# Optimization experiments

Measured on AMD Instinct MI355X. Metric: run time of the kernel, lower is better.

Reference implementation:

```python
import jax, jax.numpy as jnp
import numpy as np

EMBED_DIM = 1024
HEADS = 16
HEAD_DIM = EMBED_DIM // HEADS


def setup_inputs() -> dict:
    key = jax.random.key(0)
    ks = jax.random.split(key, 9)
    B, T, C = 4, 4096, EMBED_DIM
    s = 1.0 / np.sqrt(C)
    inp = {
        "x": jax.random.normal(ks[0], (B, T, C), dtype=jnp.float32),
        "Wq": jax.random.normal(ks[1], (C, C), dtype=jnp.float32) * s,
        "bq": jnp.zeros((C,), dtype=jnp.float32),
        "Wk": jax.random.normal(ks[2], (C, C), dtype=jnp.float32) * s,
        "bk": jnp.zeros((C,), dtype=jnp.float32),
        "Wv": jax.random.normal(ks[3], (C, C), dtype=jnp.float32) * s,
        "bv": jnp.zeros((C,), dtype=jnp.float32),
        "Wc": jax.random.normal(ks[4], (C, C), dtype=jnp.float32) * s,
        "bc": jnp.zeros((C,), dtype=jnp.float32),
    }
    return inp


def reference(x, Wq, bq, Wk, bk, Wv, bv, Wc, bc):
    B, T, C = x.shape
    H, D = HEADS, HEAD_DIM
    # projections (torch Linear: x @ W.T + b)
    q = (x @ Wq.T + bq).reshape(B, T, H, D).transpose(0, 2, 1, 3)  # [B,H,T,D]
    k = (x @ Wk.T + bk).reshape(B, T, H, D).transpose(0, 2, 1, 3)
    v = (x @ Wv.T + bv).reshape(B, T, H, D).transpose(0, 2, 1, 3)
    # ELU+1 feature map
    q = jax.nn.elu(q) + 1.0
    k = jax.nn.elu(k) + 1.0
    # kv outer product: [B,H,D,D]
    kv = jnp.einsum("bhtd,bhte->bhde", k, v)
    # normalizer: q @ sum_t k  -> [B,H,T,1]
    k_sum = k.sum(axis=2)  # [B,H,D]
    z = 1.0 / (jnp.einsum("bhtd,bhd->bht", q, k_sum)[..., None] + 1e-6)
    y = jnp.einsum("bhtd,bhde->bhte", q, kv) * z  # [B,H,T,D]
    y = y.transpose(0, 2, 1, 3).reshape(B, T, C)
    return y @ Wc.T + bc
```

## Files before the change

kernel.cpp:

```cpp
#include <hip/hip_runtime.h>
#include <math.h>

#define EMBED 1024
#define HEADS 16
#define HD 64
#define BATCH 4
#define TSEQ 4096
#define BH (BATCH * HEADS)
#define MROWS (BATCH * TSEQ)

typedef _Float16 f16;
typedef __attribute__((ext_vector_type(4))) _Float16 f16x4;
typedef __attribute__((ext_vector_type(8))) _Float16 f16x8;
typedef __attribute__((ext_vector_type(4))) float f32x4;

#define GLOBAL_AS __attribute__((address_space(1)))
#define LDS_AS __attribute__((address_space(3)))

__device__ __forceinline__ float elu1(float v) {
    return v > 0.f ? v + 1.f : __expf(v);
}

__device__ __forceinline__ int swzc(int row, int col, int cols) {
    int g = (col >> 3) ^ (row & 7);
    return row * cols + (g << 3) + (col & 7);
}

__device__ __forceinline__ f16x8 fragld(const f16* t, int row, int k, int cols) {
    return *(const f16x8*)&t[swzc(row, k, cols)];
}

__device__ __forceinline__ f32x4 mfma16(f16x8 a, f16x8 b, f32x4 c) {
    return __builtin_amdgcn_mfma_f32_16x16x32_f16(a, b, c, 0, 0, 0);
}

__device__ __forceinline__ void gld_lds16(const f16* g, f16* l) {
    __builtin_amdgcn_global_load_lds((const GLOBAL_AS void*)g, (LDS_AS void*)l, 16, 0, 0);
}

__global__ __launch_bounds__(256) void prep(
    const float* __restrict__ x, f16* __restrict__ xh,
    const float* __restrict__ Wq, const float* __restrict__ Wk,
    const float* __restrict__ Wv, const float* __restrict__ Wc,
    const float* __restrict__ bq, const float* __restrict__ bk,
    const float* __restrict__ bv, const float* __restrict__ bc,
    f16* __restrict__ Wall, float* __restrict__ ball, float* __restrict__ kvz)
{
    int bid = blockIdx.x;
    if (bid < 16384) {
        size_t i4 = (size_t)bid * 256 + threadIdx.x;
        float4 f = *(const float4*)&x[i4 * 4];
        f16x4 h = {(f16)f.x, (f16)f.y, (f16)f.z, (f16)f.w};
        *(f16x4*)&xh[i4 * 4] = h;
    } else {
        int i4 = (bid - 16384) * 256 + threadIdx.x;
        int cls = i4 >> 18;
        const float* W = cls == 0 ? Wq : cls == 1 ? Wk : cls == 2 ? Wv : Wc;
        int off = (i4 & 0x3FFFF) * 4;
        float4 f = *(const float4*)&W[off];
        f16x4 h = {(f16)f.x, (f16)f.y, (f16)f.z, (f16)f.w};
        *(f16x4*)&Wall[(size_t)i4 * 4] = h;
        if (i4 < 4096) {
            int c2 = i4 >> 10;
            const float* bb = c2 == 0 ? bq : c2 == 1 ? bk : c2 == 2 ? bv : bc;
            ball[i4] = bb[i4 & 1023];
        }
        if (i4 < 66560) {
            *(float4*)&kvz[i4 * 4] = (float4){0.f, 0.f, 0.f, 0.f};
        }
    }
}

__global__ __launch_bounds__(256) void gemm_kv(
    const f16* __restrict__ xh, const f16* __restrict__ Wall,
    const float* __restrict__ ball,
    float* __restrict__ kvg, float* __restrict__ ksg)
{
    __shared__ __align__(16) f16 smem[2 * 128 * 64];
    f16* As = smem;
    f16* Bs = smem + 128 * 64;

    const int tid = threadIdx.x, lane = tid & 63, w = tid >> 6;
    const int wr = w >> 1, wc4 = w & 1, l15 = lane & 15, l4 = lane >> 4;

    const int m0 = blockIdx.x * 128;
    const int h = blockIdx.y;

    const int gcol = ((lane & 7) ^ (lane >> 3)) << 3;
    const int rsub = lane >> 3;
    const size_t arow = (size_t)(m0 + w * 32 + rsub) * EMBED + gcol;

    const int wrow = w * 32 + rsub;
    const int brow_idx = (wrow < 64) ? (1024 + h * 64 + wrow)
                                     : (2048 + h * 64 + (wrow - 64));
    const size_t brow = (size_t)brow_idx * EMBED + gcol;

    f32x4 acc[4][4];
    #pragma unroll
    for (int i = 0; i < 4; ++i)
        #pragma unroll
        for (int j = 0; j < 4; ++j) acc[i][j] = (f32x4){0.f, 0.f, 0.f, 0.f};

    for (int k0 = 0; k0 < EMBED; k0 += 64) {
        #pragma unroll
        for (int c = 0; c < 4; ++c) {
            gld_lds16(&xh[arow + (size_t)c * 8 * EMBED + k0], &As[(w * 4 + c) * 512]);
            gld_lds16(&Wall[brow + (size_t)c * 8 * EMBED + k0], &Bs[(w * 4 + c) * 512]);
        }
        __syncthreads();
        #pragma unroll
        for (int kk = 0; kk < 64; kk += 32) {
            f16x8 af[4], bf[4];
            #pragma unroll
            for (int i = 0; i < 4; ++i)
                af[i] = fragld(As, wr * 64 + i * 16 + l15, kk + l4 * 8, 64);
            #pragma unroll
            for (int j = 0; j < 4; ++j)
                bf[j] = fragld(Bs, wc4 * 64 + j * 16 + l15, kk + l4 * 8, 64);
            #pragma unroll
            for (int i = 0; i < 4; ++i)
                #pragma unroll
                for (int j = 0; j < 4; ++j)
                    acc[i][j] = mfma16(af[i], bf[j], acc[i][j]);
        }
        __syncthreads();
    }

    f16* kt = As;
    f16* vt = Bs;
    const float* biasp = ball + (wc4 ? 2048 : 1024) + h * 64;
    #pragma unroll
    for (int j = 0; j < 4; ++j) {
        int d = j * 16 + l15;
        float bj = biasp[d];
        f16* dst = wc4 ? vt : kt;
        #pragma unroll
        for (int i = 0; i < 4; ++i) {
            int t0 = wr * 64 + i * 16 + l4 * 4;
            f16x4 hv;
            #pragma unroll
            for (int r = 0; r < 4; ++r) {
                float vv = acc[i][j][r] + bj;
                if (!wc4) vv = elu1(vv);
                hv[r] = (f16)vv;
            }
            *(f16x4*)&dst[swzc(d, t0, 128)] = hv;
        }
    }
    __syncthreads();

    f32x4 kvacc[4];
    #pragma unroll
    for (int j = 0; j < 4; ++j) kvacc[j] = (f32x4){0.f, 0.f, 0.f, 0.f};
    #pragma unroll
    for (int tc = 0; tc < 4; ++tc) {
        f16x8 a = fragld(vt, 16 * w + l15, tc * 32 + l4 * 8, 128);
        #pragma unroll
        for (int j = 0; j < 4; ++j) {
            f16x8 bfr = fragld(kt, j * 16 + l15, tc * 32 + l4 * 8, 128);
            kvacc[j] = mfma16(a, bfr, kvacc[j]);
        }
    }
    float ksacc = 0.f;
    {
        int d = tid & 63, q4 = tid >> 6;
        #pragma unroll
        for (int t8 = 0; t8 < 32; t8 += 8) {
            f16x8 k8 = fragld(kt, d, q4 * 32 + t8, 128);
            #pragma unroll
            for (int e = 0; e < 8; ++e) ksacc += (float)k8[e];
        }
    }
    const int bh = (m0 >> 12) * HEADS + h;
    #pragma unroll
    for (int j = 0; j < 4; ++j)
        #pragma unroll
        for (int r = 0; r < 4; ++r)
            atomicAdd(&kvg[(size_t)bh * 4096 +
                           (size_t)(16 * w + l4 * 4 + r) * HD + j * 16 + l15],
                      kvacc[j][r]);
    atomicAdd(&ksg[bh * HD + (tid & 63)], ksacc);
}

__global__ __launch_bounds__(256) void gemm_qy(
    const f16* __restrict__ xh, const f16* __restrict__ Wall,
    const float* __restrict__ ball,
    const float* __restrict__ kvg, const float* __restrict__ ksg,
    f16* __restrict__ y)
{
    __shared__ __align__(16) f16 smem[2 * 128 * 64];
    __shared__ __align__(16) f16 kvs[2][64 * 64];
    __shared__ float kss[2][64];
    __shared__ float zs[128][2];
    f16* As = smem;
    f16* Bs = smem + 128 * 64;

    const int tid = threadIdx.x, lane = tid & 63, w = tid >> 6;
    const int wr = w >> 1, wc4 = w & 1, l15 = lane & 15, l4 = lane >> 4;

    const int m0 = blockIdx.x * 128;
    const int ny = blockIdx.y;
    const int n0 = ny * 128;
    const int bh0 = (m0 >> 12) * HEADS + 2 * ny;

    const int gcol = ((lane & 7) ^ (lane >> 3)) << 3;
    const int rsub = lane >> 3;
    const size_t arow = (size_t)(m0 + w * 32 + rsub) * EMBED + gcol;
    const size_t brow = (size_t)(n0 + w * 32 + rsub) * EMBED + gcol;

    f32x4 acc[4][4];
    #pragma unroll
    for (int i = 0; i < 4; ++i)
        #pragma unroll
        for (int j = 0; j < 4; ++j) acc[i][j] = (f32x4){0.f, 0.f, 0.f, 0.f};

    for (int k0 = 0; k0 < EMBED; k0 += 64) {
        #pragma unroll
        for (int c = 0; c < 4; ++c) {
            gld_lds16(&xh[arow + (size_t)c * 8 * EMBED + k0], &As[(w * 4 + c) * 512]);
            gld_lds16(&Wall[brow + (size_t)c * 8 * EMBED + k0], &Bs[(w * 4 + c) * 512]);
        }
        __syncthreads();
        #pragma unroll
        for (int kk = 0; kk < 64; kk += 32) {
            f16x8 af[4], bf[4];
            #pragma unroll
            for (int i = 0; i < 4; ++i)
                af[i] = fragld(As, wr * 64 + i * 16 + l15, kk + l4 * 8, 64);
            #pragma unroll
            for (int j = 0; j < 4; ++j)
                bf[j] = fragld(Bs, wc4 * 64 + j * 16 + l15, kk + l4 * 8, 64);
            #pragma unroll
            for (int i = 0; i < 4; ++i)
                #pragma unroll
                for (int j = 0; j < 4; ++j)
                    acc[i][j] = mfma16(af[i], bf[j], acc[i][j]);
        }
        __syncthreads();
    }

    #pragma unroll
    for (int c = 0; c < 8; ++c) {
        int idx = tid + c * 256;
        int hh = idx >> 10;
        int rem = idx & 1023;
        int e = rem >> 4, d4 = (rem & 15) << 2;
        float4 f = *(const float4*)&kvg[(size_t)(bh0 + hh) * 4096 + e * 64 + d4];
        f16x4 hv = {(f16)f.x, (f16)f.y, (f16)f.z, (f16)f.w};
        *(f16x4*)&kvs[hh][swzc(e, d4, 64)] = hv;
    }
    if (tid < 128) kss[tid >> 6][tid & 63] = ksg[(bh0 + (tid >> 6)) * HD + (tid & 63)];

    #pragma unroll
    for (int j = 0; j < 4; ++j) {
        int c = wc4 * 64 + j * 16 + l15;
        float bj = ball[n0 + c];
        #pragma unroll
        for (int i = 0; i < 4; ++i) {
            #pragma unroll
            for (int r = 0; r < 4; ++r) {
                int t = wr * 64 + i * 16 + l4 * 4 + r;
                smem[swzc(t, c, 128)] = (f16)elu1(acc[i][j][r] + bj);
            }
        }
    }
    __syncthreads();

    {
        int t = tid >> 1, hh = tid & 1;
        float s = 0.f;
        #pragma unroll
        for (int d8 = 0; d8 < 64; d8 += 8) {
            f16x8 qv = fragld(smem, t, hh * 64 + d8, 128);
            #pragma unroll
            for (int e = 0; e < 8; ++e) s += (float)qv[e] * kss[hh][d8 + e];
        }
        zs[t][hh] = 1.f / (s + 1e-6f);
    }

    const int hh = w >> 1;
    const int eh = (w & 1) * 32;
    f32x4 yacc[2][8];
    #pragma unroll
    for (int et = 0; et < 2; ++et)
        #pragma unroll
        for (int jn = 0; jn < 8; ++jn) yacc[et][jn] = (f32x4){0.f, 0.f, 0.f, 0.f};
    #pragma unroll
    for (int kk = 0; kk < 64; kk += 32) {
        f16x8 a0 = fragld(kvs[hh], eh + l15, kk + l4 * 8, 64);
        f16x8 a1 = fragld(kvs[hh], eh + 16 + l15, kk + l4 * 8, 64);
        #pragma unroll
        for (int jn = 0; jn < 8; ++jn) {
            f16x8 bq8 = fragld(smem, jn * 16 + l15, hh * 64 + kk + l4 * 8, 128);
            yacc[0][jn] = mfma16(a0, bq8, yacc[0][jn]);
            yacc[1][jn] = mfma16(a1, bq8, yacc[1][jn]);
        }
    }
    __syncthreads();

    #pragma unroll
    for (int et = 0; et < 2; ++et) {
        #pragma unroll
        for (int jn = 0; jn < 8; ++jn) {
            int t = jn * 16 + l15;
            float z = zs[t][hh];
            int c0 = hh * 64 + eh + et * 16 + l4 * 4;
            f16x4 hv;
            #pragma unroll
            for (int r = 0; r < 4; ++r) hv[r] = (f16)(yacc[et][jn][r] * z);
            *(f16x4*)&smem[swzc(t, c0, 128)] = hv;
        }
    }
    __syncthreads();

    #pragma unroll
    for (int p = 0; p < 8; ++p) {
        int idx = tid + p * 256;
        int row = idx >> 4, g8 = (idx & 15) << 3;
        f16x8 v = *(const f16x8*)&smem[swzc(row, g8, 128)];
        *(f16x8*)&y[(size_t)(m0 + row) * EMBED + n0 + g8] = v;
    }
}

__global__ __launch_bounds__(256) void gemm_out(
    const f16* __restrict__ y, const f16* __restrict__ Wall,
    const float* __restrict__ ball, float* __restrict__ out)
{
    __shared__ __align__(16) f16 As[128 * 64];
    __shared__ __align__(16) f16 Bs[128 * 64];

    const int tid = threadIdx.x, lane = tid & 63, w = tid >> 6;
    const int wr = w >> 1, wc4 = w & 1, l15 = lane & 15, l4 = lane >> 4;
    const int m0 = blockIdx.x * 128;
    const int n0 = blockIdx.y * 128;

    const int gcol = ((lane & 7) ^ (lane >> 3)) << 3;
    const int rsub = lane >> 3;
    const size_t arow = (size_t)(m0 + w * 32 + rsub) * EMBED + gcol;
    const size_t brow = (size_t)(3072 + n0 + w * 32 + rsub) * EMBED + gcol;

    f32x4 acc[4][4];
    #pragma unroll
    for (int i = 0; i < 4; ++i)
        #pragma unroll
        for (int j = 0; j < 4; ++j) acc[i][j] = (f32x4){0.f, 0.f, 0.f, 0.f};

    for (int k0 = 0; k0 < EMBED; k0 += 64) {
        #pragma unroll
        for (int c = 0; c < 4; ++c) {
            gld_lds16(&y[arow + (size_t)c * 8 * EMBED + k0], &As[(w * 4 + c) * 512]);
            gld_lds16(&Wall[brow + (size_t)c * 8 * EMBED + k0], &Bs[(w * 4 + c) * 512]);
        }
        __syncthreads();
        #pragma unroll
        for (int kk = 0; kk < 64; kk += 32) {
            f16x8 af[4], bf[4];
            #pragma unroll
            for (int i = 0; i < 4; ++i)
                af[i] = fragld(As, wr * 64 + i * 16 + l15, kk + l4 * 8, 64);
            #pragma unroll
            for (int j = 0; j < 4; ++j)
                bf[j] = fragld(Bs, wc4 * 64 + j * 16 + l15, kk + l4 * 8, 64);
            #pragma unroll
            for (int i = 0; i < 4; ++i)
                #pragma unroll
                for (int j = 0; j < 4; ++j)
                    acc[i][j] = mfma16(af[i], bf[j], acc[i][j]);
        }
        __syncthreads();
    }

    #pragma unroll
    for (int j = 0; j < 4; ++j) {
        int n = n0 + wc4 * 64 + j * 16 + l15;
        float bj = ball[3072 + n];
        #pragma unroll
        for (int i = 0; i < 4; ++i) {
            #pragma unroll
            for (int r = 0; r < 4; ++r) {
                int m = m0 + wr * 64 + i * 16 + l4 * 4 + r;
                out[(size_t)m * EMBED + n] = acc[i][j][r] + bj;
            }
        }
    }
}

extern "C" void kernel_launch(void* const* d_in, const int* in_sizes, int n_in,
                              void* d_out, int out_size, void* d_ws, size_t ws_size,
                              hipStream_t stream) {
    (void)in_sizes; (void)n_in; (void)out_size; (void)ws_size;
    const float* x  = (const float*)d_in[0];
    const float* Wq = (const float*)d_in[1];
    const float* bq = (const float*)d_in[2];
    const float* Wk = (const float*)d_in[3];
    const float* bk = (const float*)d_in[4];
    const float* Wv = (const float*)d_in[5];
    const float* bv = (const float*)d_in[6];
    const float* Wc = (const float*)d_in[7];
    const float* bc = (const float*)d_in[8];
    float* out = (float*)d_out;

    char* W = (char*)d_ws;
    f16* xh   = (f16*)W;
    f16* y_ws = (f16*)(W + 33554432);
    f16* Wall = (f16*)(W + 67108864);
    float* ball = (float*)(W + 75497472);
    float* kvg  = (float*)(W + 75513856);
    float* ksg  = (float*)(W + 76562432);

    prep<<<20480, 256, 0, stream>>>(x, xh, Wq, Wk, Wv, Wc, bq, bk, bv, bc,
                                    Wall, ball, kvg);

    gemm_kv<<<dim3(128, 16), 256, 0, stream>>>(xh, Wall, ball, kvg, ksg);

    gemm_qy<<<dim3(128, 8), 256, 0, stream>>>(xh, Wall, ball, kvg, ksg, y_ws);

    gemm_out<<<dim3(128, 8), 256, 0, stream>>>(y_ws, Wall, ball, out);
}
```

Baseline: 216.6 us.

## Software-pipeline GEMM main loops with double/triple-buffered async LDS loads

Replaces the load-sync-compute-sync loop in the three GEMM kernels with a shared macro. It prefetches A tiles one step ahead into a double buffer and B tiles two steps ahead into a triple buffer, using per-wave vmcnt waits and a single barrier per iteration. The aim is to overlap global-to-LDS traffic with MFMA work and halve barrier count. LDS per block grows to about 80 KB, which reduces how many blocks can sit on a CU, and the epilogue scratch in gemm_qy is remapped onto the pipeline buffers.

Measured after the change: 226.0 us. +4.3%, slower.

```diff
diff --git a/kernel.cpp b/kernel.cpp
--- a/kernel.cpp
+++ b/kernel.cpp
@@ -37,6 +37,48 @@
 __device__ __forceinline__ void gld_lds16(const f16* g, f16* l) {
     __builtin_amdgcn_global_load_lds((const GLOBAL_AS void*)g, (LDS_AS void*)l, 16, 0, 0);
 }
+
+#define ISSUE_A(buf, kt_)                                                      \
+    _Pragma("unroll") for (int c = 0; c < 4; ++c)                              \
+        gld_lds16(&aglob[arow + (size_t)c * 8 * EMBED + (kt_) * 64],           \
+                  &(buf)[(w * 4 + c) * 512]);
+#define ISSUE_B(buf, kt_)                                                      \
+    _Pragma("unroll") for (int c = 0; c < 4; ++c)                              \
+        gld_lds16(&bglob[brow + (size_t)c * 8 * EMBED + (kt_) * 64],           \
+                  &(buf)[(w * 4 + c) * 512]);
+
+#define PIPE128_LOOP()                                                         \
+    _Pragma("unroll") for (int i = 0; i < 4; ++i)                              \
+        _Pragma("unroll") for (int j = 0; j < 4; ++j)                          \
+            acc[i][j] = (f32x4){0.f, 0.f, 0.f, 0.f};                           \
+    ISSUE_A(As[0], 0);                                                         \
+    __builtin_amdgcn_sched_barrier(0);                                         \
+    ISSUE_B(Bs[0], 0);                                                         \
+    __builtin_amdgcn_sched_barrier(0);                                         \
+    ISSUE_B(Bs[1], 1);                                                         \
+    __builtin_amdgcn_sched_barrier(0);                                         \
+    for (int kt = 0; kt < 16; ++kt) {                                          \
+        if (kt < 15) asm volatile("s_waitcnt vmcnt(4)" ::: "memory");          \
+        else         asm volatile("s_waitcnt vmcnt(0)" ::: "memory");          \
+        __builtin_amdgcn_s_barrier();                                          \
+        __builtin_amdgcn_sched_barrier(0);                                     \
+        if (kt < 15) { ISSUE_A(As[(kt + 1) & 1], kt + 1); }                    \
+        __builtin_amdgcn_sched_barrier(0);                                     \
+        if (kt < 14) { ISSUE_B(Bs[(kt + 2) % 3], kt + 2); }                    \
+        __builtin_amdgcn_sched_barrier(0);                                     \
+        const f16* cA = As[kt & 1];                                            \
+        const f16* cB = Bs[kt % 3];                                            \
+        _Pragma("unroll") for (int kk = 0; kk < 64; kk += 32) {                \
+            f16x8 af[4], bf[4];                                                \
+            _Pragma("unroll") for (int i = 0; i < 4; ++i)                      \
+                af[i] = fragld(cA, wr * 64 + i * 16 + l15, kk + l4 * 8, 64);   \
+            _Pragma("unroll") for (int j = 0; j < 4; ++j)                      \
+                bf[j] = fragld(cB, wc4 * 64 + j * 16 + l15, kk + l4 * 8, 64);  \
+            _Pragma("unroll") for (int i = 0; i < 4; ++i)                      \
+                _Pragma("unroll") for (int j = 0; j < 4; ++j)                  \
+                    acc[i][j] = mfma16(af[i], bf[j], acc[i][j]);               \
+        }                                                                      \
+    }
 
 __global__ __launch_bounds__(256) void prep(
     const float* __restrict__ x, f16* __restrict__ xh,
@@ -76,9 +118,8 @@
     const float* __restrict__ ball,
     float* __restrict__ kvg, float* __restrict__ ksg)
 {
-    __shared__ __align__(16) f16 smem[2 * 128 * 64];
-    f16* As = smem;
-    f16* Bs = smem + 128 * 64;
+    __shared__ __align__(16) f16 As[2][8192];
+    __shared__ __align__(16) f16 Bs[3][8192];
 
     const int tid = threadIdx.x, lane = tid & 63, w = tid >> 6;
     const int wr = w >> 1, wc4 = w & 1, l15 = lane & 15, l4 = lane >> 4;
@@ -88,46 +129,20 @@
 
     const int gcol = ((lane & 7) ^ (lane >> 3)) << 3;
     const int rsub = lane >> 3;
+    const f16* aglob = xh;
+    const f16* bglob = Wall;
     const size_t arow = (size_t)(m0 + w * 32 + rsub) * EMBED + gcol;
-
     const int wrow = w * 32 + rsub;
     const int brow_idx = (wrow < 64) ? (1024 + h * 64 + wrow)
                                      : (2048 + h * 64 + (wrow - 64));
     const size_t brow = (size_t)brow_idx * EMBED + gcol;
 
     f32x4 acc[4][4];
-    #pragma unroll
-    for (int i = 0; i < 4; ++i)
-        #pragma unroll
-        for (int j = 0; j < 4; ++j) acc[i][j] = (f32x4){0.f, 0.f, 0.f, 0.f};
-
-    for (int k0 = 0; k0 < EMBED; k0 += 64) {
-        #pragma unroll
-        for (int c = 0; c < 4; ++c) {
-            gld_lds16(&xh[arow + (size_t)c * 8 * EMBED + k0], &As[(w * 4 + c) * 512]);
-            gld_lds16(&Wall[brow + (size_t)c * 8 * EMBED + k0], &Bs[(w * 4 + c) * 512]);
-        }
-        __syncthreads();
-        #pragma unroll
-        for (int kk = 0; kk < 64; kk += 32) {
-            f16x8 af[4], bf[4];
-            #pragma unroll
-            for (int i = 0; i < 4; ++i)
-                af[i] = fragld(As, wr * 64 + i * 16 + l15, kk + l4 * 8, 64);
-            #pragma unroll
-            for (int j = 0; j < 4; ++j)
-                bf[j] = fragld(Bs, wc4 * 64 + j * 16 + l15, kk + l4 * 8, 64);
-            #pragma unroll
-            for (int i = 0; i < 4; ++i)
-                #pragma unroll
-                for (int j = 0; j < 4; ++j)
-                    acc[i][j] = mfma16(af[i], bf[j], acc[i][j]);
-        }
-        __syncthreads();
-    }
-
-    f16* kt = As;
-    f16* vt = Bs;
+    PIPE128_LOOP()
+    __syncthreads();
+
+    f16* kt = &As[0][0];
+    f16* vt = &As[1][0];
     const float* biasp = ball + (wc4 ? 2048 : 1024) + h * 64;
     #pragma unroll
     for (int j = 0; j < 4; ++j) {
@@ -188,12 +203,8 @@
     const float* __restrict__ kvg, const float* __restrict__ ksg,
     f16* __restrict__ y)
 {
-    __shared__ __align__(16) f16 smem[2 * 128 * 64];
-    __shared__ __align__(16) f16 kvs[2][64 * 64];
-    __shared__ float kss[2][64];
-    __shared__ float zs[128][2];
-    f16* As = smem;
-    f16* Bs = smem + 128 * 64;
+    __shared__ __align__(16) f16 As[2][8192];
+    __shared__ __align__(16) f16 Bs[3][8192];
 
     const int tid = threadIdx.x, lane = tid & 63, w = tid >> 6;
     const int wr = w >> 1, wc4 = w & 1, l15 = lane & 15, l4 = lane >> 4;
@@ -205,39 +216,19 @@
 
     const int gcol = ((lane & 7) ^ (lane >> 3)) << 3;
     const int rsub = lane >> 3;
+    const f16* aglob = xh;
+    const f16* bglob = Wall;
     const size_t arow = (size_t)(m0 + w * 32 + rsub) * EMBED + gcol;
     const size_t brow = (size_t)(n0 + w * 32 + rsub) * EMBED + gcol;
 
     f32x4 acc[4][4];
-    #pragma unroll
-    for (int i = 0; i < 4; ++i)
-        #pragma unroll
-        for (int j = 0; j < 4; ++j) acc[i][j] = (f32x4){0.f, 0.f, 0.f, 0.f};
-
-    for (int k0 = 0; k0 < EMBED; k0 += 64) {
-        #pragma unroll
-        for (int c = 0; c < 4; ++c) {
-            gld_lds16(&xh[arow + (size_t)c * 8 * EMBED + k0], &As[(w * 4 + c) * 512]);
-            gld_lds16(&Wall[brow + (size_t)c * 8 * EMBED + k0], &Bs[(w * 4 + c) * 512]);
-        }
-        __syncthreads();
-        #pragma unroll
-        for (int kk = 0; kk < 64; kk += 32) {
-            f16x8 af[4], bf[4];
-            #pragma unroll
-            for (int i = 0; i < 4; ++i)
-                af[i] = fragld(As, wr * 64 + i * 16 + l15, kk + l4 * 8, 64);
-            #pragma unroll
-            for (int j = 0; j < 4; ++j)
-                bf[j] = fragld(Bs, wc4 * 64 + j * 16 + l15, kk + l4 * 8, 64);
-            #pragma unroll
-            for (int i = 0; i < 4; ++i)
-                #pragma unroll
-                for (int j = 0; j < 4; ++j)
-                    acc[i][j] = mfma16(af[i], bf[j], acc[i][j]);
-        }
-        __syncthreads();
-    }
+    PIPE128_LOOP()
+    __syncthreads();
+
+    f16* qtile = &As[0][0];
+    f16* kvsb  = &Bs[2][0];
+    float* zs  = (float*)&Bs[0][0];
+    float* kss = zs + 256;
 
     #pragma unroll
     for (int c = 0; c < 8; ++c) {
@@ -247,9 +238,9 @@
         int e = rem >> 4, d4 = (rem & 15) << 2;
         float4 f = *(const float4*)&kvg[(size_t)(bh0 + hh) * 4096 + e * 64 + d4];
         f16x4 hv = {(f16)f.x, (f16)f.y, (f16)f.z, (f16)f.w};
-        *(f16x4*)&kvs[hh][swzc(e, d4, 64)] = hv;
-    }
-    if (tid < 128) kss[tid >> 6][tid & 63] = ksg[(bh0 + (tid >> 6)) * HD + (tid & 63)];
+        *(f16x4*)&kvsb[hh * 4096 + swzc(e, d4, 64)] = hv;
+    }
+    if (tid < 128) kss[tid] = ksg[(bh0 + (tid >> 6)) * HD + (tid & 63)];
 
     #pragma unroll
     for (int j = 0; j < 4; ++j) {
@@ -260,7 +251,7 @@
             #pragma unroll
             for (int r = 0; r < 4; ++r) {
                 int t = wr * 64 + i * 16 + l4 * 4 + r;
-                smem[swzc(t, c, 128)] = (f16)elu1(acc[i][j][r] + bj);
+                qtile[swzc(t, c, 128)] = (f16)elu1(acc[i][j][r] + bj);
             }
         }
     }
@@ -271,11 +262,11 @@
         float s = 0.f;
         #pragma unroll
         for (int d8 = 0; d8 < 64; d8 += 8) {
-            f16x8 qv = fragld(smem, t, hh * 64 + d8, 128);
-            #pragma unroll
-            for (int e = 0; e < 8; ++e) s += (float)qv[e] * kss[hh][d8 + e];
-        }
-        zs[t][hh] = 1.f / (s + 1e-6f);
+            f16x8 qv = fragld(qtile, t, hh * 64 + d8, 128);
+            #pragma unroll
+            for (int e = 0; e < 8; ++e) s += (float)qv[e] * kss[hh * 64 + d8 + e];
+        }
+        zs[t * 2 + hh] = 1.f / (s + 1e-6f);
     }
 
     const int hh = w >> 1;
@@ -287,11 +278,11 @@
         for (int jn = 0; jn < 8; ++jn) yacc[et][jn] = (f32x4){0.f, 0.f, 0.f, 0.f};
     #pragma unroll
     for (int kk = 0; kk < 64; kk += 32) {
-        f16x8 a0 = fragld(kvs[hh], eh + l15, kk + l4 * 8, 64);
-        f16x8 a1 = fragld(kvs[hh], eh + 16 + l15, kk + l4 * 8, 64);
+        f16x8 a0 = fragld(&kvsb[hh * 4096], eh + l15, kk + l4 * 8, 64);
+        f16x8 a1 = fragld(&kvsb[hh * 4096], eh + 16 + l15, kk + l4 * 8, 64);
         #pragma unroll
         for (int jn = 0; jn < 8; ++jn) {
-            f16x8 bq8 = fragld(smem, jn * 16 + l15, hh * 64 + kk + l4 * 8, 128);
+            f16x8 bq8 = fragld(qtile, jn * 16 + l15, hh * 64 + kk + l4 * 8, 128);
             yacc[0][jn] = mfma16(a0, bq8, yacc[0][jn]);
             yacc[1][jn] = mfma16(a1, bq8, yacc[1][jn]);
         }
@@ -303,12 +294,12 @@
         #pragma unroll
         for (int jn = 0; jn < 8; ++jn) {
             int t = jn * 16 + l15;
-            float z = zs[t][hh];
+            float z = zs[t * 2 + hh];
             int c0 = hh * 64 + eh + et * 16 + l4 * 4;
             f16x4 hv;
             #pragma unroll
             for (int r = 0; r < 4; ++r) hv[r] = (f16)(yacc[et][jn][r] * z);
-            *(f16x4*)&smem[swzc(t, c0, 128)] = hv;
+            *(f16x4*)&qtile[swzc(t, c0, 128)] = hv;
         }
     }
     __syncthreads();
@@ -317,7 +308,7 @@
     for (int p = 0; p < 8; ++p) {
         int idx = tid + p * 256;
         int row = idx >> 4, g8 = (idx & 15) << 3;
-        f16x8 v = *(const f16x8*)&smem[swzc(row, g8, 128)];
+        f16x8 v = *(const f16x8*)&qtile[swzc(row, g8, 128)];
         *(f16x8*)&y[(size_t)(m0 + row) * EMBED + n0 + g8] = v;
     }
 }
@@ -326,8 +317,8 @@
     const f16* __restrict__ y, const f16* __restrict__ Wall,
     const float* __restrict__ ball, float* __restrict__ out)
 {
-    __shared__ __align__(16) f16 As[128 * 64];
-    __shared__ __align__(16) f16 Bs[128 * 64];
+    __shared__ __align__(16) f16 As[2][8192];
+    __shared__ __align__(16) f16 Bs[3][8192];
 
     const int tid = threadIdx.x, lane = tid & 63, w = tid >> 6;
     const int wr = w >> 1, wc4 = w & 1, l15 = lane & 15, l4 = lane >> 4;
@@ -336,39 +327,13 @@
 
     const int gcol = ((lane & 7) ^ (lane >> 3)) << 3;
     const int rsub = lane >> 3;
+    const f16* aglob = y;
+    const f16* bglob = Wall;
     const size_t arow = (size_t)(m0 + w * 32 + rsub) * EMBED + gcol;
     const size_t brow = (size_t)(3072 + n0 + w * 32 + rsub) * EMBED + gcol;
 
     f32x4 acc[4][4];
-    #pragma unroll
-    for (int i = 0; i < 4; ++i)
-        #pragma unroll
-        for (int j = 0; j < 4; ++j) acc[i][j] = (f32x4){0.f, 0.f, 0.f, 0.f};
-
-    for (int k0 = 0; k0 < EMBED; k0 += 64) {
-        #pragma unroll
-        for (int c = 0; c < 4; ++c) {
-            gld_lds16(&y[arow + (size_t)c * 8 * EMBED + k0], &As[(w * 4 + c) * 512]);
-            gld_lds16(&Wall[brow + (size_t)c * 8 * EMBED + k0], &Bs[(w * 4 + c) * 512]);
-        }
-        __syncthreads();
-        #pragma unroll
-        for (int kk = 0; kk < 64; kk += 32) {
-            f16x8 af[4], bf[4];
-            #pragma unroll
-            for (int i = 0; i < 4; ++i)
-                af[i] = fragld(As, wr * 64 + i * 16 + l15, kk + l4 * 8, 64);
-            #pragma unroll
-            for (int j = 0; j < 4; ++j)
-                bf[j] = fragld(Bs, wc4 * 64 + j * 16 + l15, kk + l4 * 8, 64);
-            #pragma unroll
-            for (int i = 0; i < 4; ++i)
-                #pragma unroll
-                for (int j = 0; j < 4; ++j)
-                    acc[i][j] = mfma16(af[i], bf[j], acc[i][j]);
-        }
-        __syncthreads();
-    }
+    PIPE128_LOOP()
 
     #pragma unroll
     for (int j = 0; j < 4; ++j) {
```
